# Optimization experiments

Hardware: AMD Instinct MI355X
Metric: run time of the kernel (lower is better)

The kernel has to match this reference:

```python
import jax, jax.numpy as jnp
import numpy as np

N = 50000       # nodes
E = 1600000     # edges (avg degree 32)
DIN = 64
DOUT = 64
DE = 16
ATT_SLOPE = 0.2   # leaky_relu slope inside attention (GAT standard)
ACT_SLOPE = 0.01  # F.leaky_relu default between layers


def setup_inputs() -> dict:
    key = jax.random.key(0)
    ks = jax.random.split(key, 16)

    def lin(k, i, o):
        return jax.random.normal(k, (i, o), jnp.float32) / np.sqrt(i).astype(np.float32)

    def vec(k, d):
        return jax.random.normal(k, (d,), jnp.float32) / np.sqrt(d).astype(np.float32)

    return {
        "X": jax.random.normal(ks[0], (N, DIN), jnp.float32),
        "edge_index": jax.random.randint(ks[1], (2, E), 0, N),
        "edge_attr": jax.random.normal(ks[2], (E, DE), jnp.float32),
        # layer 1 params
        "W1": lin(ks[3], DIN, DOUT), "We1": lin(ks[4], DE, DOUT),
        "as1": vec(ks[5], DOUT), "ad1": vec(ks[6], DOUT), "ae1": vec(ks[7], DOUT),
        "b1": jnp.zeros((DOUT,), jnp.float32),
        # layer 2 params
        "W2": lin(ks[8], DOUT, DOUT), "We2": lin(ks[9], DE, DOUT),
        "as2": vec(ks[10], DOUT), "ad2": vec(ks[11], DOUT), "ae2": vec(ks[12], DOUT),
        "b2": jnp.zeros((DOUT,), jnp.float32),
    }


def _gat_conv(x, src, dst, edge_attr, W, We, a_s, a_d, a_e, b):
    """GATConv with edge features, softmax attention over dst neighborhoods, max aggregation."""
    n = x.shape[0]
    h = x @ W                      # [N, DOUT]
    e = edge_attr @ We             # [E, DOUT]
    # per-edge attention logits
    logits = jax.nn.leaky_relu((h @ a_s)[src] + (h @ a_d)[dst] + e @ a_e, ATT_SLOPE)  # [E]
    # numerically-stable segment softmax over destination node
    m = jax.ops.segment_max(logits, dst, num_segments=n)      # [N]
    p = jnp.exp(logits - m[dst])                               # [E]
    s = jax.ops.segment_sum(p, dst, num_segments=n)            # [N]
    att = p / jnp.maximum(s[dst], 1e-16)                       # [E]
    msg = (h[src] + e) * att[:, None]                          # [E, DOUT]
    out = jax.ops.segment_max(msg, dst, num_segments=n)        # [N, DOUT], -inf for empty
    out = jnp.where(jnp.isfinite(out), out, 0.0)
    return out + b


def reference(X, edge_index, edge_attr,
              W1, We1, as1, ad1, ae1, b1,
              W2, We2, as2, ad2, ae2, b2):
    src, dst = edge_index[0], edge_index[1]
    c1 = _gat_conv(X, src, dst, edge_attr, W1, We1, as1, ad1, ae1, b1)
    c1 = jax.nn.leaky_relu(c1, ACT_SLOPE)
    c2 = _gat_conv(c1, src, dst, edge_attr, W2, We2, as2, ad2, ae2, b2)
    c2 = jax.nn.leaky_relu(c2, ACT_SLOPE)
    return c2
```

## Files before the change

### kernel.cpp

```cpp
#include <hip/hip_runtime.h>
#include <cstdint>
#include <cstddef>

#define NN 50000
#define EE 1600000
#define D  64
#define DE 16

typedef __attribute__((ext_vector_type(2))) float vf2;

__device__ __forceinline__ float bf2f(unsigned short u) {
    return __uint_as_float(((unsigned)u) << 16);
}
__device__ __forceinline__ unsigned short f2bf(float f) {
    unsigned u = __float_as_uint(f);
    unsigned r = u + 0x7FFFu + ((u >> 16) & 1u);
    return (unsigned short)(r >> 16);
}

__global__ __launch_bounds__(256) void k_hist(const int* dst, int* counts) {
    int e = blockIdx.x * 256 + threadIdx.x;
    if (e < EE) atomicAdd(&counts[dst[e]], 1);
}

__global__ __launch_bounds__(256) void k_scanA(const int* counts, int* bsum) {
    __shared__ int tmp[256];
    int t = threadIdx.x, i = blockIdx.x * 256 + t;
    tmp[t] = (i < NN) ? counts[i] : 0;
    __syncthreads();
    for (int off = 128; off; off >>= 1) {
        if (t < off) tmp[t] += tmp[t + off];
        __syncthreads();
    }
    if (t == 0) bsum[blockIdx.x] = tmp[0];
}

__global__ __launch_bounds__(256) void k_scanB(int* bsum, int nchunks) {
    __shared__ int tmp[256];
    int t = threadIdx.x;
    int v = (t < nchunks) ? bsum[t] : 0;
    tmp[t] = v; __syncthreads();
    for (int off = 1; off < 256; off <<= 1) {
        int x = (t >= off) ? tmp[t - off] : 0;
        __syncthreads();
        tmp[t] += x;
        __syncthreads();
    }
    if (t < nchunks) bsum[t] = tmp[t] - v;
}

__global__ __launch_bounds__(256) void k_scanC(const int* counts, const int* bsumex,
                                               int* offsets, int* cursor) {
    __shared__ int tmp[256];
    int t = threadIdx.x, i = blockIdx.x * 256 + t;
    int v = (i < NN) ? counts[i] : 0;
    tmp[t] = v; __syncthreads();
    for (int off = 1; off < 256; off <<= 1) {
        int x = (t >= off) ? tmp[t - off] : 0;
        __syncthreads();
        tmp[t] += x;
        __syncthreads();
    }
    int excl = tmp[t] - v + bsumex[blockIdx.x];
    if (i < NN) { offsets[i] = excl; cursor[i] = excl; }
}

__global__ __launch_bounds__(256) void k_scatter(const int* src, const int* dst,
                                                 const float* ea,
                                                 const float* We1, const float* ae1,
                                                 const float* We2, const float* ae2,
                                                 int* cursor, int4* recs) {
    __shared__ float wsh[32];
    int t = threadIdx.x;
    if (t < 32) {
        const float* We = (t < 16) ? We1 : We2;
        const float* ae = (t < 16) ? ae1 : ae2;
        int k = t & 15;
        float acc = 0.f;
        #pragma unroll
        for (int c = 0; c < 64; c++) acc += We[k * 64 + c] * ae[c];
        wsh[t] = acc;
    }
    __syncthreads();
    float w1r[16], w2r[16];
    #pragma unroll
    for (int j = 0; j < 16; j++) { w1r[j] = wsh[j]; w2r[j] = wsh[16 + j]; }

    int e = blockIdx.x * 256 + t;
    if (e >= EE) return;
    int d = dst[e];
    const float4* rp = (const float4*)(ea + (size_t)e * DE);
    float4 q0 = rp[0], q1 = rp[1], q2 = rp[2], q3 = rp[3];
    float ev[16] = {q0.x, q0.y, q0.z, q0.w, q1.x, q1.y, q1.z, q1.w,
                    q2.x, q2.y, q2.z, q2.w, q3.x, q3.y, q3.z, q3.w};
    float e1 = 0.f, e2 = 0.f;
    #pragma unroll
    for (int j = 0; j < 16; j++) {
        e1 += ev[j] * w1r[j];
        e2 += ev[j] * w2r[j];
    }
    int pos = atomicAdd(&cursor[d], 1);
    recs[pos] = make_int4(src[e], e, __float_as_int(e1), __float_as_int(e2));
}

template<int IN_BF16>
__global__ __launch_bounds__(256, 4) void k_gemm(const void* xin, const float* W,
                                                 const float* a_s, const float* a_d,
                                                 unsigned short* h, float* hs, float* hd) {
    int t = threadIdx.x, lane = t & 63;
    int wid0 = blockIdx.x * 4 + (t >> 6);
    float Wcol[64];
    #pragma unroll
    for (int k = 0; k < 64; k++) Wcol[k] = W[k * 64 + lane];
    float asl = a_s[lane], adl = a_d[lane];
    for (int n0 = wid0; n0 < NN; n0 += 4096) {
        int n = __builtin_amdgcn_readfirstlane(n0);
        float acc = 0.f;
        if (IN_BF16) {
            const uint4* xr = (const uint4*)((const unsigned short*)xin + (size_t)n * 64);
            #pragma unroll
            for (int q = 0; q < 8; q++) {
                uint4 u = xr[q];
                unsigned uu[4] = {u.x, u.y, u.z, u.w};
                #pragma unroll
                for (int j = 0; j < 4; j++) {
                    acc += bf2f((unsigned short)(uu[j] & 0xFFFFu)) * Wcol[q * 8 + 2 * j];
                    acc += bf2f((unsigned short)(uu[j] >> 16))     * Wcol[q * 8 + 2 * j + 1];
                }
            }
        } else {
            const float4* xr = (const float4*)((const float*)xin + (size_t)n * 64);
            #pragma unroll
            for (int q = 0; q < 16; q++) {
                float4 u = xr[q];
                acc += u.x * Wcol[4 * q]     + u.y * Wcol[4 * q + 1]
                     + u.z * Wcol[4 * q + 2] + u.w * Wcol[4 * q + 3];
            }
        }
        h[(size_t)n * 64 + lane] = f2bf(acc);
        float ps = acc * asl, pd = acc * adl;
        #pragma unroll
        for (int off = 32; off; off >>= 1) {
            ps += __shfl_xor(ps, off);
            pd += __shfl_xor(pd, off);
        }
        if (lane == 0) { hs[n] = ps; hd[n] = pd; }
    }
}

template<int L2>
__global__ __launch_bounds__(256, 3) void k_gat(const int4* __restrict__ recs,
                                                const int* __restrict__ offsets,
                                                const int* __restrict__ counts,
                                                const float* __restrict__ hs,
                                                const float* __restrict__ hd,
                                                const unsigned short* __restrict__ h,
                                                const float* __restrict__ ea,
                                                const float* __restrict__ We,
                                                const float* __restrict__ b,
                                                void* __restrict__ outv) {
    __shared__ float4 eal[4][4][64];
    __shared__ float2 arx[4][64];
    int t = threadIdx.x, lane = t & 63, wv = t >> 6;
    int g = lane >> 4, cl = lane & 15;

    vf2 Wp[32];
    #pragma unroll
    for (int kp = 0; kp < 8; kp++) {
        float4 wa = *(const float4*)(We + (2 * kp) * 64 + 4 * cl);
        float4 wb = *(const float4*)(We + (2 * kp + 1) * 64 + 4 * cl);
        Wp[kp].x      = wa.x; Wp[kp].y      = wb.x;
        Wp[8 + kp].x  = wa.y; Wp[8 + kp].y  = wb.y;
        Wp[16 + kp].x = wa.z; Wp[16 + kp].y = wb.z;
        Wp[24 + kp].x = wa.w; Wp[24 + kp].y = wb.w;
    }

    int d = blockIdx.x * 4 + wv;
    int start = offsets[d];
    int deg = counts[d];

    if (deg == 0) {
        if (g == 0) {
            float4 bl = *(const float4*)(b + 4 * cl);
            float o0 = (bl.x >= 0.f) ? bl.x : 0.01f * bl.x;
            float o1 = (bl.y >= 0.f) ? bl.y : 0.01f * bl.y;
            float o2 = (bl.z >= 0.f) ? bl.z : 0.01f * bl.z;
            float o3 = (bl.w >= 0.f) ? bl.w : 0.01f * bl.w;
            size_t oidx = (size_t)d * D + 4 * cl;
            if (L2) *(float4*)((float*)outv + oidx) = make_float4(o0, o1, o2, o3);
            else {
                ushort4 ov = {f2bf(o0), f2bf(o1), f2bf(o2), f2bf(o3)};
                *(ushort4*)((unsigned short*)outv + oidx) = ov;
            }
        }
        return;
    }

    float hdv = hd[d];
    bool fast = (deg <= 64);
    float m, invs;

    float ninf = -__builtin_inff();
    float a0 = ninf, a1 = ninf, a2 = ninf, a3 = ninf;

    if (fast) {
        float lg = ninf;
        if (lane < deg) {
            int4 r = recs[start + lane];
            const float4* ep = (const float4*)(ea + (size_t)r.y * DE);
            float4 q0 = ep[0], q1 = ep[1], q2 = ep[2], q3 = ep[3];
            eal[wv][0][lane] = q0; eal[wv][1][lane] = q1;
            eal[wv][2][lane] = q2; eal[wv][3][lane] = q3;
            arx[wv][lane].y = __int_as_float(r.x);
            float ee = __int_as_float(L2 ? r.w : r.z);
            lg = hs[r.x] + hdv + ee;
            lg = (lg >= 0.f) ? lg : 0.2f * lg;
        }

        bool vC = (g < deg);
        int jC = vC ? g : 0;
        int rxC = __float_as_int(arx[wv][jC].y);
        ushort4 hvC = *(const ushort4*)(h + (size_t)rxC * D + 4 * cl);

        m = lg;
        #pragma unroll
        for (int off = 32; off; off >>= 1) m = fmaxf(m, __shfl_xor(m, off));
        float p = __expf(lg - m);
        float s = p;
        #pragma unroll
        for (int off = 32; off; off >>= 1) s += __shfl_xor(s, off);
        invs = 1.0f / fmaxf(s, 1e-16f);
        if (lane < deg) arx[wv][lane].x = p * invs;

        float attC = arx[wv][jC].x;

        for (int i = 0; i < deg; i += 4) {
            int jn = i + 4 + g;
            bool vN = (jn < deg);
            int jN = vN ? jn : 0;
            float2 arN = arx[wv][jN];
            int rxN = __float_as_int(arN.y);
            ushort4 hvN = *(const ushort4*)(h + (size_t)rxN * D + 4 * cl);

            vf2 acA = {0.f, 0.f}, acB = {0.f, 0.f}, acC = {0.f, 0.f}, acD = {0.f, 0.f};
            #pragma unroll
            for (int kq = 0; kq < 4; kq++) {
                float4 q = eal[wv][kq][jC];
                vf2 eA; eA.x = q.x; eA.y = q.y;
                vf2 eB; eB.x = q.z; eB.y = q.w;
                acA += eA * Wp[2 * kq];      acA += eB * Wp[2 * kq + 1];
                acB += eA * Wp[8 + 2 * kq];  acB += eB * Wp[8 + 2 * kq + 1];
                acC += eA * Wp[16 + 2 * kq]; acC += eB * Wp[16 + 2 * kq + 1];
                acD += eA * Wp[24 + 2 * kq]; acD += eB * Wp[24 + 2 * kq + 1];
            }
            float e0 = acA.x + acA.y, e1 = acB.x + acB.y;
            float e2 = acC.x + acC.y, e3 = acD.x + acD.y;
            float o0 = (bf2f(hvC.x) + e0) * attC;
            float o1 = (bf2f(hvC.y) + e1) * attC;
            float o2 = (bf2f(hvC.z) + e2) * attC;
            float o3 = (bf2f(hvC.w) + e3) * attC;
            if (vC) {
                a0 = fmaxf(a0, o0); a1 = fmaxf(a1, o1);
                a2 = fmaxf(a2, o2); a3 = fmaxf(a3, o3);
            }
            attC = arN.x; hvC = hvN; vC = vN; jC = jN;
        }
    } else {
        float mm = ninf, s = 0.f;
        for (int i = lane; i < deg; i += 64) {
            int4 r = recs[start + i];
            float ee = __int_as_float(L2 ? r.w : r.z);
            float lg = hs[r.x] + hdv + ee;
            lg = (lg >= 0.f) ? lg : 0.2f * lg;
            float mn = fmaxf(mm, lg);
            s = ((mm == mn) ? s : s * __expf(mm - mn)) + __expf(lg - mn);
            mm = mn;
        }
        #pragma unroll
        for (int off = 32; off; off >>= 1) {
            float m2 = __shfl_xor(mm, off);
            float s2 = __shfl_xor(s, off);
            float mn = fmaxf(mm, m2);
            float sa = (mm == mn) ? s : s * __expf(mm - mn);
            float sb = (m2 == mn) ? s2 : s2 * __expf(m2 - mn);
            s = sa + sb;
            mm = mn;
        }
        m = mm;
        invs = 1.0f / fmaxf(s, 1e-16f);

        for (int i = 0; i < deg; i += 4) {
            int j = i + g;
            bool valid = (j < deg);
            int jc = valid ? j : 0;
            int4 r = recs[start + jc];
            float ee = __int_as_float(L2 ? r.w : r.z);
            float lg = hs[r.x] + hdv + ee;
            lg = (lg >= 0.f) ? lg : 0.2f * lg;
            float att = __expf(lg - m) * invs;
            const float4* ep = (const float4*)(ea + (size_t)r.y * DE);
            float4 q0 = ep[0], q1 = ep[1], q2 = ep[2], q3 = ep[3];
            ushort4 hv = *(const ushort4*)(h + (size_t)r.x * D + 4 * cl);
            float4 qs[4] = {q0, q1, q2, q3};
            vf2 acA = {0.f, 0.f}, acB = {0.f, 0.f}, acC = {0.f, 0.f}, acD = {0.f, 0.f};
            #pragma unroll
            for (int kq = 0; kq < 4; kq++) {
                float4 q = qs[kq];
                vf2 eA; eA.x = q.x; eA.y = q.y;
                vf2 eB; eB.x = q.z; eB.y = q.w;
                acA += eA * Wp[2 * kq];      acA += eB * Wp[2 * kq + 1];
                acB += eA * Wp[8 + 2 * kq];  acB += eB * Wp[8 + 2 * kq + 1];
                acC += eA * Wp[16 + 2 * kq]; acC += eB * Wp[16 + 2 * kq + 1];
                acD += eA * Wp[24 + 2 * kq]; acD += eB * Wp[24 + 2 * kq + 1];
            }
            float e0 = acA.x + acA.y, e1 = acB.x + acB.y;
            float e2 = acC.x + acC.y, e3 = acD.x + acD.y;
            float o0 = (bf2f(hv.x) + e0) * att;
            float o1 = (bf2f(hv.y) + e1) * att;
            float o2 = (bf2f(hv.z) + e2) * att;
            float o3 = (bf2f(hv.w) + e3) * att;
            if (valid) {
                a0 = fmaxf(a0, o0); a1 = fmaxf(a1, o1);
                a2 = fmaxf(a2, o2); a3 = fmaxf(a3, o3);
            }
        }
    }

    #pragma unroll
    for (int off = 16; off <= 32; off <<= 1) {
        a0 = fmaxf(a0, __shfl_xor(a0, off));
        a1 = fmaxf(a1, __shfl_xor(a1, off));
        a2 = fmaxf(a2, __shfl_xor(a2, off));
        a3 = fmaxf(a3, __shfl_xor(a3, off));
    }

    if (g == 0) {
        float4 bl = *(const float4*)(b + 4 * cl);
        float o0 = a0 + bl.x, o1 = a1 + bl.y;
        float o2 = a2 + bl.z, o3 = a3 + bl.w;
        o0 = (o0 >= 0.f) ? o0 : 0.01f * o0;
        o1 = (o1 >= 0.f) ? o1 : 0.01f * o1;
        o2 = (o2 >= 0.f) ? o2 : 0.01f * o2;
        o3 = (o3 >= 0.f) ? o3 : 0.01f * o3;
        size_t oidx = (size_t)d * D + 4 * cl;
        if (L2) {
            *(float4*)((float*)outv + oidx) = make_float4(o0, o1, o2, o3);
        } else {
            ushort4 ov = {f2bf(o0), f2bf(o1), f2bf(o2), f2bf(o3)};
            *(ushort4*)((unsigned short*)outv + oidx) = ov;
        }
    }
}

extern "C" void kernel_launch(void* const* d_in, const int* in_sizes, int n_in,
                              void* d_out, int out_size, void* d_ws, size_t ws_size,
                              hipStream_t stream) {
    const float* X   = (const float*)d_in[0];
    const int*   eix = (const int*)d_in[1];
    const float* ea  = (const float*)d_in[2];
    const float* W1  = (const float*)d_in[3];
    const float* We1 = (const float*)d_in[4];
    const float* as1 = (const float*)d_in[5];
    const float* ad1 = (const float*)d_in[6];
    const float* ae1 = (const float*)d_in[7];
    const float* b1  = (const float*)d_in[8];
    const float* W2  = (const float*)d_in[9];
    const float* We2 = (const float*)d_in[10];
    const float* as2 = (const float*)d_in[11];
    const float* ad2 = (const float*)d_in[12];
    const float* ae2 = (const float*)d_in[13];
    const float* b2  = (const float*)d_in[14];

    const int* src = eix;
    const int* dst = eix + EE;

    char* w = (char*)d_ws;
    int4* recs = (int4*)w;               w += (size_t)EE * 16;
    unsigned short* hA = (unsigned short*)w; w += (size_t)NN * D * 2;
    unsigned short* hB = (unsigned short*)w; w += (size_t)NN * D * 2;
    float* hs = (float*)w;               w += (size_t)NN * 4;
    float* hd = (float*)w;               w += (size_t)NN * 4;
    int* counts = (int*)w;               w += (size_t)NN * 4;
    int* offsets = (int*)w;              w += (size_t)NN * 4;
    int* cursor = (int*)w;               w += (size_t)NN * 4;
    int* bsum = (int*)w;                 w += 256 * 4;

    const int nchunks = (NN + 255) / 256;

    hipMemsetAsync(counts, 0, (size_t)NN * 4, stream);
    k_hist<<<EE / 256, 256, 0, stream>>>(dst, counts);
    k_scanA<<<nchunks, 256, 0, stream>>>(counts, bsum);
    k_scanB<<<1, 256, 0, stream>>>(bsum, nchunks);
    k_scanC<<<nchunks, 256, 0, stream>>>(counts, bsum, offsets, cursor);
    k_scatter<<<EE / 256, 256, 0, stream>>>(src, dst, ea, We1, ae1, We2, ae2, cursor, recs);

    k_gemm<0><<<1024, 256, 0, stream>>>(X, W1, as1, ad1, hA, hs, hd);
    k_gat<0><<<NN / 4, 256, 0, stream>>>(recs, offsets, counts, hs, hd, hA, ea, We1, b1, hB);
    k_gemm<1><<<1024, 256, 0, stream>>>(hB, W2, as2, ad2, hB, hs, hd);
    k_gat<1><<<NN / 4, 256, 0, stream>>>(recs, offsets, counts, hs, hd, hB, ea, We2, b2,
                                         (float*)d_out);
}
```

Measured before the change: 590.0 us.

## Fuse scatter with layer-1 GEMM, shrink edge records, stage neighbor rows in LDS

The edge-scatter kernel and the first-layer node GEMM are merged into one launch: the first 1024 blocks do the GEMM and the rest scatter CSR records. Records shrink from int4 to int2 (src, edge id), so the per-edge attention term is recomputed in the GAT kernel from edge_attr and a precomputed We·ae vector, now built in scanB. In the fast path, each neighbor's full bf16 h row is loaded once into swizzled LDS, and attention weights and edge features are prefetched from LDS for the next step. The aim is less scatter traffic, one fewer launch, and fewer scattered global h gathers, at the cost of more LDS per block and repeated edge-logit arithmetic.

```diff
diff --git a/kernel.cpp b/kernel.cpp
--- a/kernel.cpp
+++ b/kernel.cpp
@@ -35,7 +35,10 @@
     if (t == 0) bsum[blockIdx.x] = tmp[0];
 }
 
-__global__ __launch_bounds__(256) void k_scanB(int* bsum, int nchunks) {
+__global__ __launch_bounds__(256) void k_scanB(int* bsum, int nchunks,
+                                               const float* We1, const float* ae1,
+                                               const float* We2, const float* ae2,
+                                               float* wae) {
     __shared__ int tmp[256];
     int t = threadIdx.x;
     int v = (t < nchunks) ? bsum[t] : 0;
@@ -47,6 +50,15 @@
         __syncthreads();
     }
     if (t < nchunks) bsum[t] = tmp[t] - v;
+    if (t < 32) {
+        const float* We = (t < 16) ? We1 : We2;
+        const float* ae = (t < 16) ? ae1 : ae2;
+        int k = t & 15;
+        float acc = 0.f;
+        #pragma unroll
+        for (int c = 0; c < 64; c++) acc += We[k * 64 + c] * ae[c];
+        wae[t] = acc;
+    }
 }
 
 __global__ __launch_bounds__(256) void k_scanC(const int* counts, const int* bsumex,
@@ -65,42 +77,59 @@
     if (i < NN) { offsets[i] = excl; cursor[i] = excl; }
 }
 
-__global__ __launch_bounds__(256) void k_scatter(const int* src, const int* dst,
-                                                 const float* ea,
-                                                 const float* We1, const float* ae1,
-                                                 const float* We2, const float* ae2,
-                                                 int* cursor, int4* recs) {
-    __shared__ float wsh[32];
+template<int IN_BF16>
+__global__ __launch_bounds__(256, 4) void k_scatter_gemm(
+        const int* src, const int* dst, int* cursor, int2* recs,
+        const void* xin, const float* W, const float* a_s, const float* a_d,
+        unsigned short* h, float* hs, float* hd) {
     int t = threadIdx.x;
-    if (t < 32) {
-        const float* We = (t < 16) ? We1 : We2;
-        const float* ae = (t < 16) ? ae1 : ae2;
-        int k = t & 15;
-        float acc = 0.f;
-        #pragma unroll
-        for (int c = 0; c < 64; c++) acc += We[k * 64 + c] * ae[c];
-        wsh[t] = acc;
-    }
-    __syncthreads();
-    float w1r[16], w2r[16];
-    #pragma unroll
-    for (int j = 0; j < 16; j++) { w1r[j] = wsh[j]; w2r[j] = wsh[16 + j]; }
-
-    int e = blockIdx.x * 256 + t;
+    if (blockIdx.x < 1024) {
+        int lane = t & 63;
+        int wid0 = blockIdx.x * 4 + (t >> 6);
+        float Wcol[64];
+        #pragma unroll
+        for (int k = 0; k < 64; k++) Wcol[k] = W[k * 64 + lane];
+        float asl = a_s[lane], adl = a_d[lane];
+        for (int n0 = wid0; n0 < NN; n0 += 4096) {
+            int n = __builtin_amdgcn_readfirstlane(n0);
+            float acc = 0.f;
+            if (IN_BF16) {
+                const uint4* xr = (const uint4*)((const unsigned short*)xin + (size_t)n * 64);
+                #pragma unroll
+                for (int q = 0; q < 8; q++) {
+                    uint4 u = xr[q];
+                    unsigned uu[4] = {u.x, u.y, u.z, u.w};
+                    #pragma unroll
+                    for (int j = 0; j < 4; j++) {
+                        acc += bf2f((unsigned short)(uu[j] & 0xFFFFu)) * Wcol[q * 8 + 2 * j];
+                        acc += bf2f((unsigned short)(uu[j] >> 16))     * Wcol[q * 8 + 2 * j + 1];
+                    }
+                }
+            } else {
+                const float4* xr = (const float4*)((const float*)xin + (size_t)n * 64);
+                #pragma unroll
+                for (int q = 0; q < 16; q++) {
+                    float4 u = xr[q];
+                    acc += u.x * Wcol[4 * q]     + u.y * Wcol[4 * q + 1]
+                         + u.z * Wcol[4 * q + 2] + u.w * Wcol[4 * q + 3];
+                }
+            }
+            h[(size_t)n * 64 + lane] = f2bf(acc);
+            float ps = acc * asl, pd = acc * adl;
+            #pragma unroll
+            for (int off = 32; off; off >>= 1) {
+                ps += __shfl_xor(ps, off);
+                pd += __shfl_xor(pd, off);
+            }
+            if (lane == 0) { hs[n] = ps; hd[n] = pd; }
+        }
+        return;
+    }
+    int e = (blockIdx.x - 1024) * 256 + t;
     if (e >= EE) return;
     int d = dst[e];
-    const float4* rp = (const float4*)(ea + (size_t)e * DE);
-    float4 q0 = rp[0], q1 = rp[1], q2 = rp[2], q3 = rp[3];
-    float ev[16] = {q0.x, q0.y, q0.z, q0.w, q1.x, q1.y, q1.z, q1.w,
-                    q2.x, q2.y, q2.z, q2.w, q3.x, q3.y, q3.z, q3.w};
-    float e1 = 0.f, e2 = 0.f;
-    #pragma unroll
-    for (int j = 0; j < 16; j++) {
-        e1 += ev[j] * w1r[j];
-        e2 += ev[j] * w2r[j];
-    }
     int pos = atomicAdd(&cursor[d], 1);
-    recs[pos] = make_int4(src[e], e, __float_as_int(e1), __float_as_int(e2));
+    recs[pos] = make_int2(src[e], e);
 }
 
 template<int IN_BF16>
@@ -149,18 +178,20 @@
 }
 
 template<int L2>
-__global__ __launch_bounds__(256, 3) void k_gat(const int4* __restrict__ recs,
+__global__ __launch_bounds__(256, 3) void k_gat(const int2* __restrict__ recs,
                                                 const int* __restrict__ offsets,
                                                 const int* __restrict__ counts,
                                                 const float* __restrict__ hs,
                                                 const float* __restrict__ hd,
                                                 const unsigned short* __restrict__ h,
                                                 const float* __restrict__ ea,
+                                                const float* __restrict__ wae,
                                                 const float* __restrict__ We,
                                                 const float* __restrict__ b,
                                                 void* __restrict__ outv) {
     __shared__ float4 eal[4][4][64];
-    __shared__ float2 arx[4][64];
+    __shared__ __align__(16) unsigned short hl[4][64][64];
+    __shared__ float attl[4][64];
     int t = threadIdx.x, lane = t & 63, wv = t >> 6;
     int g = lane >> 4, cl = lane & 15;
 
@@ -173,6 +204,15 @@
         Wp[8 + kp].x  = wa.y; Wp[8 + kp].y  = wb.y;
         Wp[16 + kp].x = wa.z; Wp[16 + kp].y = wb.z;
         Wp[24 + kp].x = wa.w; Wp[24 + kp].y = wb.w;
+    }
+    float waer[16];
+    {
+        const float4* wp4 = (const float4*)(wae + L2 * 16);
+        float4 w0 = wp4[0], w1 = wp4[1], w2 = wp4[2], w3 = wp4[3];
+        waer[0]=w0.x; waer[1]=w0.y; waer[2]=w0.z; waer[3]=w0.w;
+        waer[4]=w1.x; waer[5]=w1.y; waer[6]=w1.z; waer[7]=w1.w;
+        waer[8]=w2.x; waer[9]=w2.y; waer[10]=w2.z; waer[11]=w2.w;
+        waer[12]=w3.x; waer[13]=w3.y; waer[14]=w3.z; waer[15]=w3.w;
     }
 
     int d = blockIdx.x * 4 + wv;
@@ -206,21 +246,27 @@
     if (fast) {
         float lg = ninf;
         if (lane < deg) {
-            int4 r = recs[start + lane];
-            const float4* ep = (const float4*)(ea + (size_t)r.y * DE);
+            int2 r = recs[start + lane];
+            int sr = r.x, eid = r.y;
+            const float4* ep = (const float4*)(ea + (size_t)eid * DE);
             float4 q0 = ep[0], q1 = ep[1], q2 = ep[2], q3 = ep[3];
+            const uint4* hp = (const uint4*)(h + (size_t)sr * D);
+            float hsv = hs[sr];
             eal[wv][0][lane] = q0; eal[wv][1][lane] = q1;
             eal[wv][2][lane] = q2; eal[wv][3][lane] = q3;
-            arx[wv][lane].y = __int_as_float(r.x);
-            float ee = __int_as_float(L2 ? r.w : r.z);
-            lg = hs[r.x] + hdv + ee;
+            #pragma unroll
+            for (int q = 0; q < 8; q++) {
+                uint4 hvq = hp[q];
+                *(uint4*)&hl[wv][lane][(8 * q) ^ ((lane & 7) << 3)] = hvq;
+            }
+            float ev[16] = {q0.x, q0.y, q0.z, q0.w, q1.x, q1.y, q1.z, q1.w,
+                            q2.x, q2.y, q2.z, q2.w, q3.x, q3.y, q3.z, q3.w};
+            float ee = 0.f;
+            #pragma unroll
+            for (int j = 0; j < 16; j++) ee += ev[j] * waer[j];
+            lg = hsv + hdv + ee;
             lg = (lg >= 0.f) ? lg : 0.2f * lg;
         }
-
-        bool vC = (g < deg);
-        int jC = vC ? g : 0;
-        int rxC = __float_as_int(arx[wv][jC].y);
-        ushort4 hvC = *(const ushort4*)(h + (size_t)rxC * D + 4 * cl);
 
         m = lg;
         #pragma unroll
@@ -230,46 +276,62 @@
         #pragma unroll
         for (int off = 32; off; off >>= 1) s += __shfl_xor(s, off);
         invs = 1.0f / fmaxf(s, 1e-16f);
-        if (lane < deg) arx[wv][lane].x = p * invs;
-
-        float attC = arx[wv][jC].x;
+        if (lane < deg) attl[wv][lane] = p * invs;
+
+        bool vC = (g < deg);
+        int jC = vC ? g : 0;
+        float4 qA[4];
+        #pragma unroll
+        for (int kq = 0; kq < 4; kq++) qA[kq] = eal[wv][kq][jC];
+        ushort4 hC = *(const ushort4*)&hl[wv][jC][(4 * cl) ^ ((jC & 7) << 3)];
+        float attC = attl[wv][jC];
 
         for (int i = 0; i < deg; i += 4) {
             int jn = i + 4 + g;
             bool vN = (jn < deg);
             int jN = vN ? jn : 0;
-            float2 arN = arx[wv][jN];
-            int rxN = __float_as_int(arN.y);
-            ushort4 hvN = *(const ushort4*)(h + (size_t)rxN * D + 4 * cl);
-
-            vf2 acA = {0.f, 0.f}, acB = {0.f, 0.f}, acC = {0.f, 0.f}, acD = {0.f, 0.f};
+            float4 qB[4];
+            #pragma unroll
+            for (int kq = 0; kq < 4; kq++) qB[kq] = eal[wv][kq][jN];
+            ushort4 hN = *(const ushort4*)&hl[wv][jN][(4 * cl) ^ ((jN & 7) << 3)];
+            float attN = attl[wv][jN];
+
+            vf2 acA = {0.f, 0.f}, acB = {0.f, 0.f}, acC2 = {0.f, 0.f}, acD = {0.f, 0.f};
             #pragma unroll
             for (int kq = 0; kq < 4; kq++) {
-                float4 q = eal[wv][kq][jC];
+                float4 q = qA[kq];
                 vf2 eA; eA.x = q.x; eA.y = q.y;
                 vf2 eB; eB.x = q.z; eB.y = q.w;
-                acA += eA * Wp[2 * kq];      acA += eB * Wp[2 * kq + 1];
-                acB += eA * Wp[8 + 2 * kq];  acB += eB * Wp[8 + 2 * kq + 1];
-                acC += eA * Wp[16 + 2 * kq]; acC += eB * Wp[16 + 2 * kq + 1];
-                acD += eA * Wp[24 + 2 * kq]; acD += eB * Wp[24 + 2 * kq + 1];
+                acA += eA * Wp[2 * kq];       acA += eB * Wp[2 * kq + 1];
+                acB += eA * Wp[8 + 2 * kq];   acB += eB * Wp[8 + 2 * kq + 1];
+                acC2 += eA * Wp[16 + 2 * kq]; acC2 += eB * Wp[16 + 2 * kq + 1];
+                acD += eA * Wp[24 + 2 * kq];  acD += eB * Wp[24 + 2 * kq + 1];
             }
             float e0 = acA.x + acA.y, e1 = acB.x + acB.y;
-            float e2 = acC.x + acC.y, e3 = acD.x + acD.y;
-            float o0 = (bf2f(hvC.x) + e0) * attC;
-            float o1 = (bf2f(hvC.y) + e1) * attC;
-            float o2 = (bf2f(hvC.z) + e2) * attC;
-            float o3 = (bf2f(hvC.w) + e3) * attC;
+            float e2 = acC2.x + acC2.y, e3 = acD.x + acD.y;
+            float o0 = (bf2f(hC.x) + e0) * attC;
+            float o1 = (bf2f(hC.y) + e1) * attC;
+            float o2 = (bf2f(hC.z) + e2) * attC;
+            float o3 = (bf2f(hC.w) + e3) * attC;
             if (vC) {
                 a0 = fmaxf(a0, o0); a1 = fmaxf(a1, o1);
                 a2 = fmaxf(a2, o2); a3 = fmaxf(a3, o3);
             }
-            attC = arN.x; hvC = hvN; vC = vN; jC = jN;
+            #pragma unroll
+            for (int kq = 0; kq < 4; kq++) qA[kq] = qB[kq];
+            hC = hN; attC = attN; vC = vN;
         }
     } else {
         float mm = ninf, s = 0.f;
         for (int i = lane; i < deg; i += 64) {
-            int4 r = recs[start + i];
-            float ee = __int_as_float(L2 ? r.w : r.z);
+            int2 r = recs[start + i];
+            const float4* ep = (const float4*)(ea + (size_t)r.y * DE);
+            float4 q0 = ep[0], q1 = ep[1], q2 = ep[2], q3 = ep[3];
+            float ev[16] = {q0.x, q0.y, q0.z, q0.w, q1.x, q1.y, q1.z, q1.w,
+                            q2.x, q2.y, q2.z, q2.w, q3.x, q3.y, q3.z, q3.w};
+            float ee = 0.f;
+            #pragma unroll
+            for (int j = 0; j < 16; j++) ee += ev[j] * waer[j];
             float lg = hs[r.x] + hdv + ee;
             lg = (lg >= 0.f) ? lg : 0.2f * lg;
             float mn = fmaxf(mm, lg);
@@ -293,28 +355,32 @@
             int j = i + g;
             bool valid = (j < deg);
             int jc = valid ? j : 0;
-            int4 r = recs[start + jc];
-            float ee = __int_as_float(L2 ? r.w : r.z);
+            int2 r = recs[start + jc];
+            const float4* ep = (const float4*)(ea + (size_t)r.y * DE);
+            float4 q0 = ep[0], q1 = ep[1], q2 = ep[2], q3 = ep[3];
+            float ev[16] = {q0.x, q0.y, q0.z, q0.w, q1.x, q1.y, q1.z, q1.w,
+                            q2.x, q2.y, q2.z, q2.w, q3.x, q3.y, q3.z, q3.w};
+            float ee = 0.f;
+            #pragma unroll
+            for (int j2 = 0; j2 < 16; j2++) ee += ev[j2] * waer[j2];
             float lg = hs[r.x] + hdv + ee;
             lg = (lg >= 0.f) ? lg : 0.2f * lg;
             float att = __expf(lg - m) * invs;
-            const float4* ep = (const float4*)(ea + (size_t)r.y * DE);
-            float4 q0 = ep[0], q1 = ep[1], q2 = ep[2], q3 = ep[3];
             ushort4 hv = *(const ushort4*)(h + (size_t)r.x * D + 4 * cl);
             float4 qs[4] = {q0, q1, q2, q3};
-            vf2 acA = {0.f, 0.f}, acB = {0.f, 0.f}, acC = {0.f, 0.f}, acD = {0.f, 0.f};
+            vf2 acA = {0.f, 0.f}, acB = {0.f, 0.f}, acC2 = {0.f, 0.f}, acD = {0.f, 0.f};
             #pragma unroll
             for (int kq = 0; kq < 4; kq++) {
                 float4 q = qs[kq];
                 vf2 eA; eA.x = q.x; eA.y = q.y;
                 vf2 eB; eB.x = q.z; eB.y = q.w;
-                acA += eA * Wp[2 * kq];      acA += eB * Wp[2 * kq + 1];
-                acB += eA * Wp[8 + 2 * kq];  acB += eB * Wp[8 + 2 * kq + 1];
-                acC += eA * Wp[16 + 2 * kq]; acC += eB * Wp[16 + 2 * kq + 1];
-                acD += eA * Wp[24 + 2 * kq]; acD += eB * Wp[24 + 2 * kq + 1];
+                acA += eA * Wp[2 * kq];       acA += eB * Wp[2 * kq + 1];
+                acB += eA * Wp[8 + 2 * kq];   acB += eB * Wp[8 + 2 * kq + 1];
+                acC2 += eA * Wp[16 + 2 * kq]; acC2 += eB * Wp[16 + 2 * kq + 1];
+                acD += eA * Wp[24 + 2 * kq];  acD += eB * Wp[24 + 2 * kq + 1];
             }
             float e0 = acA.x + acA.y, e1 = acB.x + acB.y;
-            float e2 = acC.x + acC.y, e3 = acD.x + acD.y;
+            float e2 = acC2.x + acC2.y, e3 = acD.x + acD.y;
             float o0 = (bf2f(hv.x) + e0) * att;
             float o1 = (bf2f(hv.y) + e1) * att;
             float o2 = (bf2f(hv.z) + e2) * att;
@@ -375,7 +441,7 @@
     const int* dst = eix + EE;
 
     char* w = (char*)d_ws;
-    int4* recs = (int4*)w;               w += (size_t)EE * 16;
+    int2* recs = (int2*)w;               w += (size_t)EE * 8;
     unsigned short* hA = (unsigned short*)w; w += (size_t)NN * D * 2;
     unsigned short* hB = (unsigned short*)w; w += (size_t)NN * D * 2;
     float* hs = (float*)w;               w += (size_t)NN * 4;
@@ -384,19 +450,22 @@
     int* offsets = (int*)w;              w += (size_t)NN * 4;
     int* cursor = (int*)w;               w += (size_t)NN * 4;
     int* bsum = (int*)w;                 w += 256 * 4;
+    float* wae = (float*)w;              w += 32 * 4;
 
     const int nchunks = (NN + 255) / 256;
+    const int nsblk = (EE + 255) / 256;
 
     hipMemsetAsync(counts, 0, (size_t)NN * 4, stream);
-    k_hist<<<EE / 256, 256, 0, stream>>>(dst, counts);
+    k_hist<<<nsblk, 256, 0, stream>>>(dst, counts);
     k_scanA<<<nchunks, 256, 0, stream>>>(counts, bsum);
-    k_scanB<<<1, 256, 0, stream>>>(bsum, nchunks);
+    k_scanB<<<1, 256, 0, stream>>>(bsum, nchunks, We1, ae1, We2, ae2, wae);
     k_scanC<<<nchunks, 256, 0, stream>>>(counts, bsum, offsets, cursor);
-    k_scatter<<<EE / 256, 256, 0, stream>>>(src, dst, ea, We1, ae1, We2, ae2, cursor, recs);
-
-    k_gemm<0><<<1024, 256, 0, stream>>>(X, W1, as1, ad1, hA, hs, hd);
-    k_gat<0><<<NN / 4, 256, 0, stream>>>(recs, offsets, counts, hs, hd, hA, ea, We1, b1, hB);
+
+    k_scatter_gemm<0><<<1024 + nsblk, 256, 0, stream>>>(src, dst, cursor, recs,
+                                                        X, W1, as1, ad1, hA, hs, hd);
+    k_gat<0><<<NN / 4, 256, 0, stream>>>(recs, offsets, counts, hs, hd, hA, ea,
+                                         wae, We1, b1, hB);
     k_gemm<1><<<1024, 256, 0, stream>>>(hB, W2, as2, ad2, hB, hs, hd);
-    k_gat<1><<<NN / 4, 256, 0, stream>>>(recs, offsets, counts, hs, hd, hB, ea, We2, b2,
-                                         (float*)d_out);
-}
+    k_gat<1><<<NN / 4, 256, 0, stream>>>(recs, offsets, counts, hs, hd, hB, ea,
+                                         wae, We2, b2, (float*)d_out);
+}
```

Measured after the change: 678.7 us. 1.15x slower.
